# Kernel tuning notes

Hardware: AMD Instinct MI355X
Metric: run time of the kernel (lower is better)

The kernel has to match this reference:

```python
import jax, jax.numpy as jnp
import numpy as np

H = 256      # hidden_size
V = 32000    # output_size (vocab)
L = 2048     # encoder max_len
B = 64       # batch

def setup_inputs():
    key = jax.random.key(0)
    ks = jax.random.split(key, 13)
    s = 0.05
    return {
        "input": jax.random.randint(ks[0], (1, B), 0, V),
        "hidden": jax.random.normal(ks[1], (1, B, H), dtype=jnp.float32),
        "encoder_outputs": jax.random.normal(ks[2], (L, B, H), dtype=jnp.float32),
        "use_cuda": 0,
        "emb_table": jax.random.normal(ks[3], (V, H), dtype=jnp.float32) * s,
        "attn_W": jax.random.normal(ks[4], (H, 2 * H), dtype=jnp.float32) * s,
        "attn_b": jax.random.normal(ks[5], (H,), dtype=jnp.float32) * s,
        "flatten": jax.random.normal(ks[6], (1, H), dtype=jnp.float32) * s,
        "gru_Wih": jax.random.normal(ks[7], (3 * H, 2 * H), dtype=jnp.float32) * s,
        "gru_Whh": jax.random.normal(ks[8], (3 * H, H), dtype=jnp.float32) * s,
        "gru_bih": jax.random.normal(ks[9], (3 * H,), dtype=jnp.float32) * s,
        "gru_bhh": jax.random.normal(ks[10], (3 * H,), dtype=jnp.float32) * s,
        "out_W": jax.random.normal(ks[11], (V, 2 * H), dtype=jnp.float32) * s,
        "out_b": jax.random.normal(ks[12], (V,), dtype=jnp.float32) * s,
    }

def reference(input, hidden, encoder_outputs, use_cuda, emb_table, attn_W, attn_b,
              flatten, gru_Wih, gru_Whh, gru_bih, gru_bhh, out_W, out_b):
    h = hidden[0]                                   # [B, H]
    embedded = emb_table[input[0]]                  # [B, H]; dropout is identity at eval
    # Bahdanau energies, vectorized: e[b,l] = flatten . (attn_W @ [h_b; enc_{l,b}] + attn_b)
    fvec = flatten[0]                               # [H]
    w = attn_W.T @ fvec                             # [2H]; split contributions of h and enc
    bias_term = fvec @ attn_b                       # scalar
    e_h = h @ w[:H]                                 # [B]
    e_enc = jnp.einsum('lbh,h->bl', encoder_outputs, w[H:])  # [B, L]
    energies = e_enc + e_h[:, None] + bias_term
    attn_weights = jax.nn.softmax(energies, axis=1)           # [B, L]
    context = jnp.einsum('bl,lbh->bh', attn_weights, encoder_outputs)  # [B, H]
    # one GRU step on x = [embedded; context] (PyTorch gate order r, z, n)
    x = jnp.concatenate([embedded, context], axis=1)          # [B, 2H]
    gi = x @ gru_Wih.T + gru_bih                              # [B, 3H]
    gh = h @ gru_Whh.T + gru_bhh                              # [B, 3H]
    r = jax.nn.sigmoid(gi[:, :H] + gh[:, :H])
    z = jax.nn.sigmoid(gi[:, H:2 * H] + gh[:, H:2 * H])
    n = jnp.tanh(gi[:, 2 * H:] + r * gh[:, 2 * H:])
    h_new = (1.0 - z) * n + z * h                             # [B, H]
    logits = jnp.concatenate([h_new, context], axis=1) @ out_W.T + out_b  # [B, V]
    output = jax.nn.log_softmax(logits, axis=-1)
    return output, h_new[None], attn_weights[:, None, :]
```

## Files before the change

kernel.cpp:

```cpp
#include <hip/hip_runtime.h>
#include <math.h>

#define H 256
#define V 32000
#define L 2048
#define B 64
#define NCH 16

#define WS_W      0
#define WS_BIAS   512
#define WS_EH     513
#define WS_ENERGY 640
#define WS_PART   (640 + B*L)
#define WS_XCAT   (WS_PART + NCH*B*H)
#define WS_M      (WS_XCAT + B*2*H)
#define WS_S      (WS_M + B)

__global__ __launch_bounds__(512) void k1_prep(
    const float* __restrict__ attn_W, const float* __restrict__ attn_b,
    const float* __restrict__ flatten, const float* __restrict__ hidden,
    float* __restrict__ ws) {
  __shared__ float fv[H];
  __shared__ float w_s[2 * H];
  __shared__ float red[H];
  int tid = threadIdx.x;
  if (tid < H) fv[tid] = flatten[tid];
  __syncthreads();
  float acc = 0.f;
  for (int hh = 0; hh < H; ++hh) acc += attn_W[hh * 2 * H + tid] * fv[hh];
  w_s[tid] = acc;
  ws[WS_W + tid] = acc;
  if (tid < H) red[tid] = fv[tid] * attn_b[tid];
  __syncthreads();
  for (int s = H / 2; s > 0; s >>= 1) {
    if (tid < s) red[tid] += red[tid + s];
    __syncthreads();
  }
  if (tid == 0) ws[WS_BIAS] = red[0];
  if (tid < B) {
    float a = 0.f;
    for (int h = 0; h < H; ++h) a += hidden[tid * H + h] * w_s[h];
    ws[WS_EH + tid] = a;
  }
}

__global__ __launch_bounds__(256) void k2_energy(
    const float* __restrict__ enc, float* __restrict__ ws) {
  int tid = threadIdx.x;
  int lane = tid & 63;
  size_t pair = (size_t)blockIdx.x * 4 + (tid >> 6);
  const float4* e4 = (const float4*)enc;
  float4 e = e4[pair * (H / 4) + lane];
  float4 w2 = ((const float4*)(ws + WS_W + H))[lane];
  float v = e.x * w2.x + e.y * w2.y + e.z * w2.z + e.w * w2.w;
  for (int off = 32; off > 0; off >>= 1) v += __shfl_xor(v, off, 64);
  if (lane == 0) {
    int b = (int)(pair & (B - 1));
    int l = (int)(pair >> 6);
    ws[WS_ENERGY + b * L + l] = v + ws[WS_EH + b] + ws[WS_BIAS];
  }
}

__global__ __launch_bounds__(256) void k3_softmax(
    const float* __restrict__ ws, float* __restrict__ d_out) {
  int b = blockIdx.x, tid = threadIdx.x;
  __shared__ float red[256];
  float e[L / 256];
  float m = -INFINITY;
#pragma unroll
  for (int i = 0; i < L / 256; ++i) {
    e[i] = ws[WS_ENERGY + b * L + i * 256 + tid];
    m = fmaxf(m, e[i]);
  }
  red[tid] = m;
  __syncthreads();
  for (int s = 128; s > 0; s >>= 1) {
    if (tid < s) red[tid] = fmaxf(red[tid], red[tid + s]);
    __syncthreads();
  }
  m = red[0];
  __syncthreads();
  float s0 = 0.f;
#pragma unroll
  for (int i = 0; i < L / 256; ++i) {
    e[i] = expf(e[i] - m);
    s0 += e[i];
  }
  red[tid] = s0;
  __syncthreads();
  for (int s = 128; s > 0; s >>= 1) {
    if (tid < s) red[tid] += red[tid + s];
    __syncthreads();
  }
  float inv = 1.f / red[0];
  float* aw = d_out + (size_t)B * V + (size_t)B * H + (size_t)b * L;
#pragma unroll
  for (int i = 0; i < L / 256; ++i) aw[i * 256 + tid] = e[i] * inv;
}

__global__ __launch_bounds__(256) void k4_ctx(
    const float* __restrict__ enc, const float* __restrict__ d_out_r,
    float* __restrict__ ws) {
  int b = blockIdx.x, ch = blockIdx.y, tid = threadIdx.x;
  const float* aw = d_out_r + (size_t)B * V + (size_t)B * H + (size_t)b * L;
  float acc = 0.f;
  int l0 = ch * (L / NCH);
  for (int i = 0; i < L / NCH; ++i) {
    int l = l0 + i;
    acc += aw[l] * enc[((size_t)l * B + b) * H + tid];
  }
  ws[WS_PART + (size_t)(ch * B + b) * H + tid] = acc;
}

__global__ __launch_bounds__(256) void k5_gru(
    const int* __restrict__ input, const float* __restrict__ hidden,
    const float* __restrict__ emb, const float* __restrict__ Wih,
    const float* __restrict__ Whh, const float* __restrict__ bih,
    const float* __restrict__ bhh, float* __restrict__ ws,
    float* __restrict__ d_out) {
  int b = blockIdx.x, tid = threadIdx.x;
  __shared__ float x_s[2 * H];
  __shared__ float h_s[H];
  __shared__ float gi_s[3 * H];
  __shared__ float gh_s[3 * H];
  float c = 0.f;
#pragma unroll
  for (int ch = 0; ch < NCH; ++ch) c += ws[WS_PART + (size_t)(ch * B + b) * H + tid];
  int tok = input[b];
  x_s[tid] = emb[(size_t)tok * H + tid];
  x_s[H + tid] = c;
  h_s[tid] = hidden[b * H + tid];
  __syncthreads();
#pragma unroll
  for (int j0 = 0; j0 < 3; ++j0) {
    int j = j0 * H + tid;
    const float4* wr = (const float4*)(Wih + (size_t)j * 2 * H);
    const float4* xr = (const float4*)x_s;
    float gi = bih[j];
#pragma unroll 4
    for (int k = 0; k < 2 * H / 4; ++k) {
      float4 wv = wr[k], xv = xr[k];
      gi += wv.x * xv.x + wv.y * xv.y + wv.z * xv.z + wv.w * xv.w;
    }
    const float4* wh = (const float4*)(Whh + (size_t)j * H);
    const float4* hr = (const float4*)h_s;
    float gh = bhh[j];
#pragma unroll 4
    for (int k = 0; k < H / 4; ++k) {
      float4 wv = wh[k], hv = hr[k];
      gh += wv.x * hv.x + wv.y * hv.y + wv.z * hv.z + wv.w * hv.w;
    }
    gi_s[j] = gi;
    gh_s[j] = gh;
  }
  __syncthreads();
  float r = 1.f / (1.f + expf(-(gi_s[tid] + gh_s[tid])));
  float z = 1.f / (1.f + expf(-(gi_s[H + tid] + gh_s[H + tid])));
  float n = tanhf(gi_s[2 * H + tid] + r * gh_s[2 * H + tid]);
  float hn = (1.f - z) * n + z * h_s[tid];
  d_out[(size_t)B * V + (size_t)b * H + tid] = hn;
  ws[WS_XCAT + (size_t)b * 2 * H + tid] = hn;
  ws[WS_XCAT + (size_t)b * 2 * H + H + tid] = c;
}

__global__ __launch_bounds__(256) void k6_logits(
    const float* __restrict__ outW, const float* __restrict__ outb,
    const float* __restrict__ ws, float* __restrict__ d_out) {
  __shared__ float As[64 * 65];
  __shared__ float Bs[64 * 65];
  int tid = threadIdx.x;
  int v0 = blockIdx.x * 64;
  int bq = tid & 15, vq = tid >> 4;
  float acc[4][4] = {{0.f}};
  const float* xc = ws + WS_XCAT;
  for (int kc = 0; kc < 8; ++kc) {
    for (int idx = tid; idx < 4096; idx += 256) {
      int r = idx >> 6, k = idx & 63;
      As[r * 65 + k] = xc[r * 512 + kc * 64 + k];
      Bs[r * 65 + k] = outW[(size_t)(v0 + r) * 512 + kc * 64 + k];
    }
    __syncthreads();
#pragma unroll 8
    for (int k = 0; k < 64; ++k) {
      float a0 = As[(bq * 4 + 0) * 65 + k];
      float a1 = As[(bq * 4 + 1) * 65 + k];
      float a2 = As[(bq * 4 + 2) * 65 + k];
      float a3 = As[(bq * 4 + 3) * 65 + k];
      float b0 = Bs[(vq * 4 + 0) * 65 + k];
      float b1 = Bs[(vq * 4 + 1) * 65 + k];
      float b2 = Bs[(vq * 4 + 2) * 65 + k];
      float b3 = Bs[(vq * 4 + 3) * 65 + k];
      acc[0][0] += a0 * b0; acc[0][1] += a0 * b1; acc[0][2] += a0 * b2; acc[0][3] += a0 * b3;
      acc[1][0] += a1 * b0; acc[1][1] += a1 * b1; acc[1][2] += a1 * b2; acc[1][3] += a1 * b3;
      acc[2][0] += a2 * b0; acc[2][1] += a2 * b1; acc[2][2] += a2 * b2; acc[2][3] += a2 * b3;
      acc[3][0] += a3 * b0; acc[3][1] += a3 * b1; acc[3][2] += a3 * b2; acc[3][3] += a3 * b3;
    }
    __syncthreads();
  }
#pragma unroll
  for (int i = 0; i < 4; ++i)
#pragma unroll
    for (int j = 0; j < 4; ++j) {
      int bb = bq * 4 + i;
      int vv = v0 + vq * 4 + j;
      d_out[(size_t)bb * V + vv] = acc[i][j] + outb[vv];
    }
}

__global__ __launch_bounds__(256) void k7_lse(
    const float* __restrict__ d_out_r, float* __restrict__ ws) {
  int b = blockIdx.x, tid = threadIdx.x;
  __shared__ float red[256];
  const float* row = d_out_r + (size_t)b * V;
  float m = -INFINITY;
  for (int i = tid; i < V; i += 256) m = fmaxf(m, row[i]);
  red[tid] = m;
  __syncthreads();
  for (int s = 128; s > 0; s >>= 1) {
    if (tid < s) red[tid] = fmaxf(red[tid], red[tid + s]);
    __syncthreads();
  }
  m = red[0];
  __syncthreads();
  float s0 = 0.f;
  for (int i = tid; i < V; i += 256) s0 += expf(row[i] - m);
  red[tid] = s0;
  __syncthreads();
  for (int s = 128; s > 0; s >>= 1) {
    if (tid < s) red[tid] += red[tid + s];
    __syncthreads();
  }
  if (tid == 0) {
    ws[WS_M + b] = m;
    ws[WS_S + b] = logf(red[0]);
  }
}

__global__ __launch_bounds__(256) void k8_norm(
    const float* __restrict__ ws, float* __restrict__ d_out) {
  int b = blockIdx.y;
  int v = blockIdx.x * 256 + threadIdx.x;
  float off = ws[WS_M + b] + ws[WS_S + b];
  d_out[(size_t)b * V + v] -= off;
}

extern "C" void kernel_launch(void* const* d_in, const int* in_sizes, int n_in,
                              void* d_out, int out_size, void* d_ws, size_t ws_size,
                              hipStream_t stream) {
  const int* input = (const int*)d_in[0];
  const float* hidden = (const float*)d_in[1];
  const float* enc = (const float*)d_in[2];
  const float* emb = (const float*)d_in[4];
  const float* attn_W = (const float*)d_in[5];
  const float* attn_b = (const float*)d_in[6];
  const float* flatten = (const float*)d_in[7];
  const float* gru_Wih = (const float*)d_in[8];
  const float* gru_Whh = (const float*)d_in[9];
  const float* gru_bih = (const float*)d_in[10];
  const float* gru_bhh = (const float*)d_in[11];
  const float* out_W = (const float*)d_in[12];
  const float* out_b = (const float*)d_in[13];
  float* out = (float*)d_out;
  float* ws = (float*)d_ws;

  k1_prep<<<1, 512, 0, stream>>>(attn_W, attn_b, flatten, hidden, ws);
  k2_energy<<<(L * B) / 4, 256, 0, stream>>>(enc, ws);
  k3_softmax<<<B, 256, 0, stream>>>(ws, out);
  k4_ctx<<<dim3(B, NCH), 256, 0, stream>>>(enc, out, ws);
  k5_gru<<<B, 256, 0, stream>>>(input, hidden, emb, gru_Wih, gru_Whh,
                                gru_bih, gru_bhh, ws, out);
  k6_logits<<<V / 64, 256, 0, stream>>>(out_W, out_b, ws, out);
  k7_lse<<<B, 256, 0, stream>>>(out, ws);
  k8_norm<<<dim3(V / 256, B), 256, 0, stream>>>(ws, out);
}
```

Baseline: 489.7 us.

## Split GRU step into wave-per-dot-product gate kernel and widen LSE reduction

The single 64-block GRU kernel is split into three kernels. One concatenates embedding and context, one computes each gate dot product with a 64-lane wavefront and shuffle reduction over 49152 (b,j) pairs, and one applies the elementwise gate math. This spreads the GRU matvec across many more CUs instead of 64 blocks, each serially streaming the whole weight matrices. The log-sum-exp kernel also moves from 256 to 1024 threads per row. The cost is two extra launches and workspace round-trips, with gate buffers reusing the energy and partial-sum regions.

```diff
diff --git a/kernel.cpp b/kernel.cpp
--- a/kernel.cpp
+++ b/kernel.cpp
@@ -11,9 +11,12 @@
 #define WS_BIAS   512
 #define WS_EH     513
 #define WS_ENERGY 640
+#define WS_GI     640
+#define WS_GH     (640 + B*3*H)
 #define WS_PART   (640 + B*L)
-#define WS_XCAT   (WS_PART + NCH*B*H)
-#define WS_M      (WS_XCAT + B*2*H)
+#define WS_XCAT2  WS_PART
+#define WS_X      (WS_PART + NCH*B*H)
+#define WS_M      (WS_X + B*2*H)
 #define WS_S      (WS_M + B)
 
 __global__ __launch_bounds__(512) void k1_prep(
@@ -112,55 +115,65 @@
   ws[WS_PART + (size_t)(ch * B + b) * H + tid] = acc;
 }
 
-__global__ __launch_bounds__(256) void k5_gru(
-    const int* __restrict__ input, const float* __restrict__ hidden,
-    const float* __restrict__ emb, const float* __restrict__ Wih,
-    const float* __restrict__ Whh, const float* __restrict__ bih,
-    const float* __restrict__ bhh, float* __restrict__ ws,
+__global__ __launch_bounds__(256) void k4b_xcat(
+    const int* __restrict__ input, const float* __restrict__ emb,
+    float* __restrict__ ws) {
+  int b = blockIdx.x, tid = threadIdx.x;
+  float c = 0.f;
+#pragma unroll
+  for (int ch = 0; ch < NCH; ++ch)
+    c += ws[WS_PART + (size_t)(ch * B + b) * H + tid];
+  int tok = input[b];
+  ws[WS_X + (size_t)b * 2 * H + tid] = emb[(size_t)tok * H + tid];
+  ws[WS_X + (size_t)b * 2 * H + H + tid] = c;
+}
+
+__global__ __launch_bounds__(256) void k5a_gates_mv(
+    const float* __restrict__ Wih, const float* __restrict__ Whh,
+    const float* __restrict__ bih, const float* __restrict__ bhh,
+    const float* __restrict__ hidden, float* __restrict__ ws) {
+  int tid = threadIdx.x, lane = tid & 63;
+  int p = blockIdx.x * 4 + (tid >> 6);
+  int j = p >> 6, b = p & 63;
+  const float4* wr = (const float4*)(Wih + (size_t)j * 2 * H);
+  const float4* xr = (const float4*)(ws + WS_X + (size_t)b * 2 * H);
+  float4 wa = wr[lane],      xa = xr[lane];
+  float4 wb = wr[64 + lane], xb = xr[64 + lane];
+  float gi = wa.x * xa.x + wa.y * xa.y + wa.z * xa.z + wa.w * xa.w
+           + wb.x * xb.x + wb.y * xb.y + wb.z * xb.z + wb.w * xb.w;
+  const float4* wh = (const float4*)(Whh + (size_t)j * H);
+  const float4* hr = (const float4*)(hidden + (size_t)b * H);
+  float4 wc = wh[lane], hc = hr[lane];
+  float gh = wc.x * hc.x + wc.y * hc.y + wc.z * hc.z + wc.w * hc.w;
+  for (int off = 32; off > 0; off >>= 1) {
+    gi += __shfl_xor(gi, off, 64);
+    gh += __shfl_xor(gh, off, 64);
+  }
+  if (lane == 0) {
+    ws[WS_GI + (size_t)b * 3 * H + j] = gi + bih[j];
+    ws[WS_GH + (size_t)b * 3 * H + j] = gh + bhh[j];
+  }
+}
+
+__global__ __launch_bounds__(256) void k5b_gates(
+    const float* __restrict__ hidden, float* __restrict__ ws,
     float* __restrict__ d_out) {
   int b = blockIdx.x, tid = threadIdx.x;
-  __shared__ float x_s[2 * H];
-  __shared__ float h_s[H];
-  __shared__ float gi_s[3 * H];
-  __shared__ float gh_s[3 * H];
-  float c = 0.f;
-#pragma unroll
-  for (int ch = 0; ch < NCH; ++ch) c += ws[WS_PART + (size_t)(ch * B + b) * H + tid];
-  int tok = input[b];
-  x_s[tid] = emb[(size_t)tok * H + tid];
-  x_s[H + tid] = c;
-  h_s[tid] = hidden[b * H + tid];
-  __syncthreads();
-#pragma unroll
-  for (int j0 = 0; j0 < 3; ++j0) {
-    int j = j0 * H + tid;
-    const float4* wr = (const float4*)(Wih + (size_t)j * 2 * H);
-    const float4* xr = (const float4*)x_s;
-    float gi = bih[j];
-#pragma unroll 4
-    for (int k = 0; k < 2 * H / 4; ++k) {
-      float4 wv = wr[k], xv = xr[k];
-      gi += wv.x * xv.x + wv.y * xv.y + wv.z * xv.z + wv.w * xv.w;
-    }
-    const float4* wh = (const float4*)(Whh + (size_t)j * H);
-    const float4* hr = (const float4*)h_s;
-    float gh = bhh[j];
-#pragma unroll 4
-    for (int k = 0; k < H / 4; ++k) {
-      float4 wv = wh[k], hv = hr[k];
-      gh += wv.x * hv.x + wv.y * hv.y + wv.z * hv.z + wv.w * hv.w;
-    }
-    gi_s[j] = gi;
-    gh_s[j] = gh;
-  }
-  __syncthreads();
-  float r = 1.f / (1.f + expf(-(gi_s[tid] + gh_s[tid])));
-  float z = 1.f / (1.f + expf(-(gi_s[H + tid] + gh_s[H + tid])));
-  float n = tanhf(gi_s[2 * H + tid] + r * gh_s[2 * H + tid]);
-  float hn = (1.f - z) * n + z * h_s[tid];
+  float gir = ws[WS_GI + (size_t)b * 3 * H + tid];
+  float giz = ws[WS_GI + (size_t)b * 3 * H + H + tid];
+  float gin = ws[WS_GI + (size_t)b * 3 * H + 2 * H + tid];
+  float ghr = ws[WS_GH + (size_t)b * 3 * H + tid];
+  float ghz = ws[WS_GH + (size_t)b * 3 * H + H + tid];
+  float ghn = ws[WS_GH + (size_t)b * 3 * H + 2 * H + tid];
+  float c = ws[WS_X + (size_t)b * 2 * H + H + tid];
+  float h = hidden[(size_t)b * H + tid];
+  float r = 1.f / (1.f + expf(-(gir + ghr)));
+  float z = 1.f / (1.f + expf(-(giz + ghz)));
+  float n = tanhf(gin + r * ghn);
+  float hn = (1.f - z) * n + z * h;
   d_out[(size_t)B * V + (size_t)b * H + tid] = hn;
-  ws[WS_XCAT + (size_t)b * 2 * H + tid] = hn;
-  ws[WS_XCAT + (size_t)b * 2 * H + H + tid] = c;
+  ws[WS_XCAT2 + (size_t)b * 2 * H + tid] = hn;
+  ws[WS_XCAT2 + (size_t)b * 2 * H + H + tid] = c;
 }
 
 __global__ __launch_bounds__(256) void k6_logits(
@@ -172,7 +185,7 @@
   int v0 = blockIdx.x * 64;
   int bq = tid & 15, vq = tid >> 4;
   float acc[4][4] = {{0.f}};
-  const float* xc = ws + WS_XCAT;
+  const float* xc = ws + WS_XCAT2;
   for (int kc = 0; kc < 8; ++kc) {
     for (int idx = tid; idx < 4096; idx += 256) {
       int r = idx >> 6, k = idx & 63;
@@ -207,26 +220,26 @@
     }
 }
 
-__global__ __launch_bounds__(256) void k7_lse(
+__global__ __launch_bounds__(1024) void k7_lse(
     const float* __restrict__ d_out_r, float* __restrict__ ws) {
   int b = blockIdx.x, tid = threadIdx.x;
-  __shared__ float red[256];
+  __shared__ float red[1024];
   const float* row = d_out_r + (size_t)b * V;
   float m = -INFINITY;
-  for (int i = tid; i < V; i += 256) m = fmaxf(m, row[i]);
+  for (int i = tid; i < V; i += 1024) m = fmaxf(m, row[i]);
   red[tid] = m;
   __syncthreads();
-  for (int s = 128; s > 0; s >>= 1) {
+  for (int s = 512; s > 0; s >>= 1) {
     if (tid < s) red[tid] = fmaxf(red[tid], red[tid + s]);
     __syncthreads();
   }
   m = red[0];
   __syncthreads();
   float s0 = 0.f;
-  for (int i = tid; i < V; i += 256) s0 += expf(row[i] - m);
+  for (int i = tid; i < V; i += 1024) s0 += expf(row[i] - m);
   red[tid] = s0;
   __syncthreads();
-  for (int s = 128; s > 0; s >>= 1) {
+  for (int s = 512; s > 0; s >>= 1) {
     if (tid < s) red[tid] += red[tid + s];
     __syncthreads();
   }
@@ -267,9 +280,11 @@
   k2_energy<<<(L * B) / 4, 256, 0, stream>>>(enc, ws);
   k3_softmax<<<B, 256, 0, stream>>>(ws, out);
   k4_ctx<<<dim3(B, NCH), 256, 0, stream>>>(enc, out, ws);
-  k5_gru<<<B, 256, 0, stream>>>(input, hidden, emb, gru_Wih, gru_Whh,
-                                gru_bih, gru_bhh, ws, out);
+  k4b_xcat<<<B, 256, 0, stream>>>(input, emb, ws);
+  k5a_gates_mv<<<(3 * H * B) / 4, 256, 0, stream>>>(gru_Wih, gru_Whh, gru_bih,
+                                                    gru_bhh, hidden, ws);
+  k5b_gates<<<B, 256, 0, stream>>>(hidden, ws, out);
   k6_logits<<<V / 64, 256, 0, stream>>>(out_W, out_b, ws, out);
-  k7_lse<<<B, 256, 0, stream>>>(out, ws);
+  k7_lse<<<B, 1024, 0, stream>>>(out, ws);
   k8_norm<<<dim3(V / 256, B), 256, 0, stream>>>(ws, out);
 }
```

New measurement: 397.1 us. -18.9%, faster.
